# Kernel tuning notes

Hardware: AMD Instinct MI355X
Metric: run time of the kernel (lower is better)

Reference implementation:

```python
import jax, jax.numpy as jnp
import numpy as np

# Dimensions (see shape_source)
B, C, H, W = 8, 3, 256, 256
WIDTH = 32   # FNO width
MODES = 12   # modes1 == modes2
L = 4        # number of FNO layers
GAP = 4      # encoder_de sample_gap
PAD = 9      # trans_net.padding


def _downsample(x):
    # Faithful vectorized form of encoder_de.output: keep indices i % GAP == 0
    # (output size int((N-1)/GAP)+1 == number of multiples of GAP below N).
    return x[:, :, ::GAP, ::GAP]


def _spectral_conv(x, w1, w2):
    # SpectralConv2d: rfft2 -> low-mode complex channel mix -> irfft2
    Hp, Wp = x.shape[-2], x.shape[-1]
    x_ft = jnp.fft.rfft2(x)  # [B, WIDTH, Hp, Wp//2+1] complex64
    out_ft = jnp.zeros((x.shape[0], w1.shape[1], Hp, Wp // 2 + 1), dtype=jnp.complex64)
    out_ft = out_ft.at[:, :, :MODES, :MODES].set(
        jnp.einsum('bixy,ioxy->boxy', x_ft[:, :, :MODES, :MODES], w1))
    out_ft = out_ft.at[:, :, -MODES:, :MODES].set(
        jnp.einsum('bixy,ioxy->boxy', x_ft[:, :, -MODES:, :MODES], w2))
    return jnp.fft.irfft2(out_ft, s=(Hp, Wp))


def _forward(x_en, fc0_w, fc0_b, w1r, w1i, w2r, w2i, pw_w, pw_b,
             fc1_w, fc1_b, fc2_w, fc2_b):
    x_de = _downsample(x_en)
    # fc0 on channels-last, back to channels-first
    x = jnp.einsum('bchw,cd->bdhw', x_en, fc0_w) + fc0_b[None, :, None, None]
    # F.pad(x, [0, PAD, 0, PAD]) pads right/bottom of last two dims
    x = jnp.pad(x, ((0, 0), (0, 0), (0, PAD), (0, PAD)))
    for l in range(L):
        w1 = (w1r[l] + 1j * w1i[l]).astype(jnp.complex64)
        w2 = (w2r[l] + 1j * w2i[l]).astype(jnp.complex64)
        x1 = _spectral_conv(x, w1, w2)
        x2 = jnp.einsum('bihw,oi->bohw', x, pw_w[l]) + pw_b[l][None, :, None, None]
        x = x1 + x2
        if l < L - 1:  # last layer has no activation
            x = jax.nn.gelu(x, approximate=False)  # torch F.gelu default = exact erf
    trans_out = x[..., :-PAD, :-PAD].transpose(0, 2, 3, 1)  # [B,H,W,WIDTH]
    h = jax.nn.gelu(trans_out @ fc1_w + fc1_b, approximate=False)  # [B,H,W,128]
    pred_delta = (h @ fc2_w + fc2_b).transpose(0, 3, 1, 2)          # [B,3,H,W]
    pred = pred_delta + x_en
    pred_de = _downsample(pred)
    return pred_de, x_de, pred, x_en


def setup_inputs() -> dict:
    key = jax.random.key(0)
    ks = jax.random.split(key, 14)
    scale = 1.0 / (WIDTH * WIDTH)
    f32 = jnp.float32
    x_en = jax.random.normal(ks[0], (B, C, H, W), f32)
    ctr = jnp.zeros((B, 1), f32)  # accepted but unused by trans_net.forward
    fc0_w = jax.random.normal(ks[1], (3, WIDTH), f32) * 0.2
    fc0_b = jnp.zeros((WIDTH,), f32)
    # torch.rand(..., dtype=cfloat): uniform [0,1) real and imag parts
    w1r = scale * jax.random.uniform(ks[2], (L, WIDTH, WIDTH, MODES, MODES), f32)
    w1i = scale * jax.random.uniform(ks[3], (L, WIDTH, WIDTH, MODES, MODES), f32)
    w2r = scale * jax.random.uniform(ks[4], (L, WIDTH, WIDTH, MODES, MODES), f32)
    w2i = scale * jax.random.uniform(ks[5], (L, WIDTH, WIDTH, MODES, MODES), f32)
    pw_w = jax.random.normal(ks[6], (L, WIDTH, WIDTH), f32) / np.sqrt(WIDTH)  # 1x1 conv [out,in]
    pw_b = jnp.zeros((L, WIDTH), f32)
    fc1_w = jax.random.normal(ks[7], (WIDTH, 128), f32) / np.sqrt(WIDTH)
    fc1_b = jnp.zeros((128,), f32)
    fc2_w = jax.random.normal(ks[8], (128, 3), f32) / np.sqrt(128.0)
    fc2_b = jnp.zeros((3,), f32)
    return dict(x_en=x_en, ctr=ctr, fc0_w=fc0_w, fc0_b=fc0_b,
                w1r=w1r, w1i=w1i, w2r=w2r, w2i=w2i,
                pw_w=pw_w, pw_b=pw_b, fc1_w=fc1_w, fc1_b=fc1_b,
                fc2_w=fc2_w, fc2_b=fc2_b)


def reference(x_en, ctr, fc0_w, fc0_b, w1r, w1i, w2r, w2i, pw_w, pw_b,
              fc1_w, fc1_b, fc2_w, fc2_b):
    del ctr  # unused in the original trans_net.forward
    return _forward(x_en, fc0_w, fc0_b, w1r, w1i, w2r, w2i, pw_w, pw_b,
                    fc1_w, fc1_b, fc2_w, fc2_b)
```

## Files before the change

kernel.cpp:

```cpp
#include <hip/hip_runtime.h>
#include <math.h>

#define HP 265
#define NPIX 70225
#define ROWF 8480
#define TWO_PI 6.28318530717958647692f

#define OFF_X     0
#define OFF_U     8988800
#define OFF_G     10752640
#define OFF_A     11342464
#define OFF_TFB   12427904
#define OFF_TS    12432512
#define OFF_W1B   12436864
#define OFF_W2B   12438912
#define OFF_PWB   12439936

typedef __attribute__((ext_vector_type(8))) short short8;
typedef __attribute__((ext_vector_type(4))) float f32x4;

__device__ __forceinline__ float gelu_f(float v){
  float x2 = v*v;
  float p  = fmaf(x2, 0.10295597f, 2.30212056f);
  float tn = -v*p;
  float e  = __builtin_amdgcn_exp2f(tn);
  float r  = __builtin_amdgcn_rcpf(1.0f + e);
  return v * r;
}
__device__ __forceinline__ unsigned short f2b(float f){
  unsigned u = __float_as_uint(f);
  u += 0x7FFFu + ((u >> 16) & 1u);
  return (unsigned short)(u >> 16);
}
__device__ __forceinline__ unsigned cvtpk(float lo, float hi){
  unsigned r;
  asm("v_cvt_pk_bf16_f32 %0, %1, %2" : "=v"(r) : "v"(lo), "v"(hi));
  return r;
}

__device__ __forceinline__ void init_body(int idx,
                       unsigned short* __restrict__ Tfb, unsigned short* __restrict__ Ts,
                       unsigned short* __restrict__ w1b, unsigned short* __restrict__ w2b,
                       unsigned short* __restrict__ pwb,
                       const float* __restrict__ fc1w, const float* __restrict__ fc2w,
                       const float* __restrict__ pw_w){
  if (idx < 32*288){
    int m = idx / 288, hc = idx % 288;
    unsigned short v = 0;
    if (m < 26 && hc < 265){
      int k = m >> 1;
      int t = (hc*k) % HP;
      float s, c; sincosf(TWO_PI*(float)t/(float)HP, &s, &c);
      v = f2b((m & 1) ? -s : c);
    }
    Tfb[idx] = v;
  }
  if (idx < 272*32){
    int w = idx >> 5, kap = idx & 31;
    unsigned short v = 0;
    if (w < HP && kap < 24){
      int k = kap >> 1;
      int t = (w*k) % HP;
      float s, c; sincosf(TWO_PI*(float)t/(float)HP, &s, &c);
      const float invN = 1.f/70225.f;
      float val = (!(kap&1)) ? invN*(k==0 ? 1.f : 2.f*c)
                             : ((k==0) ? 0.f : -invN*2.f*s);
      v = f2b(val);
    }
    Ts[idx] = v;
  }
  if (idx < 4096){
    int n = idx >> 5, k = idx & 31;
    w1b[idx] = f2b(fc1w[k*128 + n]);
  }
  if (idx < 2048){
    int n = idx >> 7, k = idx & 127;
    w2b[idx] = (n < 3) ? f2b(fc2w[k*3 + n]) : (unsigned short)0;
  }
  if (idx < 4096)
    pwb[idx] = f2b(pw_w[idx]);
}

__global__ __launch_bounds__(256) void k_fc0(const float* __restrict__ xen,
                                             const float* __restrict__ w0,
                                             const float* __restrict__ b0,
                                             unsigned short* __restrict__ xb,
                                             float* __restrict__ out,
                                             unsigned short* __restrict__ Tfb,
                                             unsigned short* __restrict__ Ts,
                                             unsigned short* __restrict__ w1b,
                                             unsigned short* __restrict__ w2b,
                                             unsigned short* __restrict__ pwb,
                                             const float* __restrict__ fc1w,
                                             const float* __restrict__ fc2w,
                                             const float* __restrict__ pw_w){
  if (blockIdx.x >= 2195){
    init_body((blockIdx.x - 2195)*256 + threadIdx.x, Tfb, Ts, w1b, w2b, pwb,
              fc1w, fc2w, pw_w);
    return;
  }
  int idx = blockIdx.x*256 + threadIdx.x;
  if (idx >= 8*NPIX) return;
  int w = idx % HP; int t = idx / HP; int h = t % HP; int b = t / HP;
  float o32[32];
  if (h < 256 && w < 256){
    const float* xp = xen + (((size_t)b*3)*256 + h)*256 + w;
    float c0 = xp[0], c1 = xp[65536], c2 = xp[131072];
    #pragma unroll
    for (int d = 0; d < 32; ++d)
      o32[d] = b0[d] + c0*w0[d] + c1*w0[32+d] + c2*w0[64+d];
    size_t be = ((size_t)b*3)*65536 + (h<<8) + w;
    out[1769472 + be]          = c0;
    out[1769472 + be + 65536]  = c1;
    out[1769472 + be + 131072] = c2;
    if (((h|w)&3) == 0){
      size_t db = ((size_t)b*3)*4096 + ((h>>2)<<6) + (w>>2);
      out[98304 + db]        = c0;
      out[98304 + db + 4096] = c1;
      out[98304 + db + 8192] = c2;
    }
  } else {
    #pragma unroll
    for (int d = 0; d < 32; ++d) o32[d] = 0.f;
  }
  uint4* dst = (uint4*)(xb + (size_t)idx*32);
  #pragma unroll
  for (int q = 0; q < 4; ++q)
    dst[q] = make_uint4(cvtpk(o32[8*q],o32[8*q+1]),   cvtpk(o32[8*q+2],o32[8*q+3]),
                        cvtpk(o32[8*q+4],o32[8*q+5]), cvtpk(o32[8*q+6],o32[8*q+7]));
}

__global__ __launch_bounds__(256) void k_dftm(const unsigned short* __restrict__ xb,
                                              const unsigned short* __restrict__ Tfb,
                                              float* __restrict__ U32){
  int tid = threadIdx.x;
  int wv = tid>>6, lane = tid&63, lr = lane&15, g = lane>>4, lk = g*8;
  int n0 = blockIdx.x*64;
  int b  = blockIdx.y;
  int n  = n0 + wv*16 + lr;
  const unsigned short* xcol = xb + (size_t)b*HP*ROWF + n;
  f32x4 acc0 = {0.f,0.f,0.f,0.f}, acc1 = {0.f,0.f,0.f,0.f};
  #pragma unroll
  for (int kc = 0; kc < 9; ++kc){
    short8 hv;
    int hb = kc*32 + lk;
    #pragma unroll
    for (int q = 0; q < 8; ++q){
      int h = hb + q;
      hv[q] = (h < HP) ? (short)xcol[(size_t)h*ROWF] : (short)0;
    }
    short8 aT0 = *(const short8*)&Tfb[lr*288 + kc*32 + lk];
    short8 aT1 = *(const short8*)&Tfb[(16+lr)*288 + kc*32 + lk];
    acc0 = __builtin_amdgcn_mfma_f32_16x16x32_bf16(aT0, hv, acc0, 0,0,0);
    acc1 = __builtin_amdgcn_mfma_f32_16x16x32_bf16(aT1, hv, acc1, 0,0,0);
  }
  if (n < 8480){
    #pragma unroll
    for (int r = 0; r < 4; ++r){
      int m0 = g*4 + r;
      U32[((size_t)b*26 + m0)*8480 + n] = acc0[r];
      int m1 = 16 + m0;
      if (m1 < 26) U32[((size_t)b*26 + m1)*8480 + n] = acc1[r];
    }
  }
}

__global__ __launch_bounds__(256) void k_spec(const float* __restrict__ U32,
                                              const float* __restrict__ w1r,
                                              const float* __restrict__ w1i,
                                              const float* __restrict__ w2r,
                                              const float* __restrict__ w2i,
                                              float2* __restrict__ G, int l){
  __shared__ float part[256*25];
  __shared__ float Xs[32*25];
  int j = blockIdx.x;
  int b = blockIdx.y;
  int ws = blockIdx.z;
  int tid = threadIdx.x;
  int wsub = tid >> 5, i = tid & 31;
  int kk   = (j < 12) ? j : (24 - j);
  bool cj  = (j >= 12);
  float xr[12], xi[12];
  #pragma unroll
  for (int k = 0; k < 12; ++k){ xr[k] = 0.f; xi[k] = 0.f; }
  const float* ubr = U32 + ((size_t)(b*26 + 2*kk))*8480;
  for (int w = ws*8 + wsub; w < HP; w += 32){
    int n = w*32 + i;
    float ux = ubr[n];
    float uy = ubr[8480 + n];
    if (cj) uy = -uy;
    float bs, bc; sincosf(-TWO_PI*(float)w/(float)HP, &bs, &bc);
    float pr = 1.f, pi = 0.f;
    #pragma unroll
    for (int k = 0; k < 12; ++k){
      xr[k] = fmaf(ux, pr, fmaf(-uy, pi, xr[k]));
      xi[k] = fmaf(ux, pi, fmaf( uy, pr, xi[k]));
      float npr = pr*bc - pi*bs;
      pi = fmaf(pr, bs, pi*bc);
      pr = npr;
    }
  }
  #pragma unroll
  for (int k = 0; k < 12; ++k){
    part[tid*25 + 2*k]     = xr[k];
    part[tid*25 + 2*k + 1] = xi[k];
  }
  __syncthreads();
  {
    int sg = tid >> 5;
    int ii = tid & 31;
    #pragma unroll
    for (int s0 = 0; s0 < 3; ++s0){
      int s = sg*3 + s0;
      float acc = 0.f;
      #pragma unroll
      for (int wq = 0; wq < 8; ++wq) acc += part[(wq*32 + ii)*25 + s];
      Xs[ii*25 + s] = acc;
    }
  }
  __syncthreads();
  int ky = (j < 12) ? j : (j - 12);
  const float* wr = (j < 12) ? w1r : w2r;
  const float* wi = (j < 12) ? w1i : w2i;
  float2* Gp = G + (size_t)ws*73728;
  for (int p = tid; p < 384; p += 256){
    int o = p / 12, kx = p % 12;
    size_t wbase = (size_t)l*147456 + (size_t)o*144 + (size_t)ky*12 + kx;
    float gr = 0.f, gi = 0.f;
    #pragma unroll 4
    for (int i2 = 0; i2 < 32; ++i2){
      float xvr = Xs[i2*25 + 2*kx];
      float xvi = Xs[i2*25 + 2*kx + 1];
      float a = wr[wbase + (size_t)i2*4608];
      float c = wi[wbase + (size_t)i2*4608];
      gr += xvr*a - xvi*c;
      gi += xvr*c + xvi*a;
    }
    Gp[((size_t)(b*32 + o)*24 + j)*12 + kx] = make_float2(gr, gi);
  }
}

__global__ __launch_bounds__(320) void k_idft_h(const float2* __restrict__ G,
                                                unsigned short* __restrict__ A16){
  __shared__ float2 gs[288];
  int bo = blockIdx.x;
  for (int i = threadIdx.x; i < 288; i += 320){
    float2 g0 = G[(size_t)bo*288 + i];
    float2 g1 = G[73728 + (size_t)bo*288 + i];
    float2 g2 = G[2*73728 + (size_t)bo*288 + i];
    float2 g3 = G[3*73728 + (size_t)bo*288 + i];
    gs[i] = make_float2(g0.x+g1.x+g2.x+g3.x, g0.y+g1.y+g2.y+g3.y);
  }
  __syncthreads();
  if (threadIdx.x >= 133) return;
  int h = blockIdx.y*133 + threadIdx.x;
  if (h >= HP) return;
  float ar[12], ai[12];
  #pragma unroll
  for (int k = 0; k < 12; ++k){ ar[k] = 0.f; ai[k] = 0.f; }
  for (int j = 0; j < 24; ++j){
    int ky = (j < 12) ? j : (241 + j);
    int t = (ky*h) % HP;
    float s, c; sincosf(TWO_PI*(float)t/(float)HP, &s, &c);
    #pragma unroll
    for (int k = 0; k < 12; ++k){
      float2 g = gs[j*12 + k];
      ar[k] = fmaf(g.x, c, fmaf(-g.y, s, ar[k]));
      ai[k] = fmaf(g.x, s, fmaf( g.y, c, ai[k]));
    }
  }
  int b = bo >> 5, o = bo & 31;
  uint4* ap = (uint4*)(A16 + (((size_t)(b*HP + h))*32 + o)*32);
  #pragma unroll
  for (int q = 0; q < 3; ++q)
    ap[q] = make_uint4(cvtpk(ar[4*q],   ai[4*q]),   cvtpk(ar[4*q+1], ai[4*q+1]),
                       cvtpk(ar[4*q+2], ai[4*q+2]), cvtpk(ar[4*q+3], ai[4*q+3]));
  ap[3] = make_uint4(0u, 0u, 0u, 0u);
}

__global__ __launch_bounds__(256) void k_final(const unsigned short* __restrict__ A16,
                                               const unsigned short* __restrict__ Tsyn,
                                               const unsigned short* __restrict__ pwb,
                                               const float* __restrict__ pw_b,
                                               unsigned short* __restrict__ xb, int l){
  int tid = threadIdx.x;
  int wv = tid>>6, lane = tid&63, lr = lane&15, g = lane>>4, lk = g*8;
  int h = blockIdx.x*4 + wv;
  int b = blockIdx.y;
  int z = blockIdx.z;
  if (h >= HP) return;
  const unsigned short* arow = A16 + (size_t)(b*HP + h)*1024;
  short8 aA0 = *(const short8*)&arow[lr*32 + lk];
  short8 aA1 = *(const short8*)&arow[(16+lr)*32 + lk];
  short8 aP0 = *(const short8*)&pwb[l*1024 + lr*32 + lk];
  short8 aP1 = *(const short8*)&pwb[l*1024 + (16+lr)*32 + lk];
  float4 vb0 = *(const float4*)&pw_b[l*32 + g*4];
  float4 vb1 = *(const float4*)&pw_b[l*32 + 16 + g*4];
  unsigned short* xrow = xb + (size_t)(b*HP + h)*ROWF;
  const f32x4 z4 = {0.f,0.f,0.f,0.f};
  const int wt0 = z ? 9 : 0, wt1 = z ? 17 : 9;
  int w = wt0*16 + lr;
  short8 bT = *(const short8*)&Tsyn[(size_t)w*32 + lk];
  short8 bX = *(const short8*)&xrow[(size_t)w*32 + lk];
  #pragma unroll
  for (int wt = wt0; wt < wt1; ++wt){
    short8 nT, nX;
    if (wt + 1 < wt1){
      int wn = (wt+1)*16 + lr;
      nT = *(const short8*)&Tsyn[(size_t)wn*32 + lk];
      nX = *(const short8*)&xrow[(size_t)wn*32 + lk];
    }
    f32x4 a0 = __builtin_amdgcn_mfma_f32_16x16x32_bf16(aA0, bT, z4, 0,0,0);
    a0 = __builtin_amdgcn_mfma_f32_16x16x32_bf16(aP0, bX, a0, 0,0,0);
    f32x4 a1 = __builtin_amdgcn_mfma_f32_16x16x32_bf16(aA1, bT, z4, 0,0,0);
    a1 = __builtin_amdgcn_mfma_f32_16x16x32_bf16(aP1, bX, a1, 0,0,0);
    if (w < HP){
      float v0[4], v1[4];
      v0[0]=a0[0]+vb0.x; v0[1]=a0[1]+vb0.y; v0[2]=a0[2]+vb0.z; v0[3]=a0[3]+vb0.w;
      v1[0]=a1[0]+vb1.x; v1[1]=a1[1]+vb1.y; v1[2]=a1[2]+vb1.z; v1[3]=a1[3]+vb1.w;
      if (l < 3){
        #pragma unroll
        for (int r = 0; r < 4; ++r){ v0[r] = gelu_f(v0[r]); v1[r] = gelu_f(v1[r]); }
      }
      *(uint2*)&xrow[(size_t)w*32 + g*4] =
          make_uint2(cvtpk(v0[0],v0[1]), cvtpk(v0[2],v0[3]));
      *(uint2*)&xrow[(size_t)w*32 + 16 + g*4] =
          make_uint2(cvtpk(v1[0],v1[1]), cvtpk(v1[2],v1[3]));
    }
    bT = nT; bX = nX; w += 16;
  }
}

__global__ __launch_bounds__(256) void k_head(const unsigned short* __restrict__ xb,
                                              const float* __restrict__ xen,
                                              const unsigned short* __restrict__ w1b,
                                              const float* __restrict__ fc1b,
                                              const unsigned short* __restrict__ w2b,
                                              const float* __restrict__ fc2b,
                                              float* __restrict__ out){
  __shared__ unsigned short Pm[4][2][16*136];
  int tid = threadIdx.x;
  int b = blockIdx.x >> 8, h = blockIdx.x & 255;
  int wv = tid>>6, lane = tid&63, lr = lane&15, g = lane>>4, lk = g*8;
  short8 bf1[8], bf2[4];
  #pragma unroll
  for (int nt = 0; nt < 8; ++nt)
    bf1[nt] = *(const short8*)&w1b[(nt*16+lr)*32 + lk];
  #pragma unroll
  for (int ks = 0; ks < 4; ++ks)
    bf2[ks] = *(const short8*)&w2b[lr*128 + ks*32 + lk];
  float f2c = (lr < 3) ? fc2b[lr] : 0.f;
  const unsigned short* xrow = xb + (size_t)(b*HP + h)*ROWF;
  const f32x4 z4 = {0.f,0.f,0.f,0.f};
  #pragma unroll
  for (int m = 0; m < 4; ++m){
    unsigned short* P = Pm[wv][m & 1];
    int p0 = (wv*4 + m)*16;
    short8 ax = *(const short8*)&xrow[(size_t)(p0 + lr)*32 + lk];
    f32x4 acc[8];
    #pragma unroll
    for (int nt = 0; nt < 8; ++nt)
      acc[nt] = __builtin_amdgcn_mfma_f32_16x16x32_bf16(bf1[nt], ax, z4, 0,0,0);
    #pragma unroll
    for (int nt = 0; nt < 8; ++nt){
      float4 bb = *(const float4*)&fc1b[nt*16 + g*4];
      float h0 = gelu_f(acc[nt][0] + bb.x);
      float h1 = gelu_f(acc[nt][1] + bb.y);
      float h2 = gelu_f(acc[nt][2] + bb.z);
      float h3 = gelu_f(acc[nt][3] + bb.w);
      *(uint2*)&P[lr*136 + nt*16 + g*4] =
          make_uint2(cvtpk(h0,h1), cvtpk(h2,h3));
    }
    f32x4 a2 = z4;
    #pragma unroll
    for (int ks = 0; ks < 4; ++ks){
      short8 ap = *(const short8*)&P[lr*136 + ks*32 + lk];
      a2 = __builtin_amdgcn_mfma_f32_16x16x32_bf16(ap, bf2[ks], a2, 0,0,0);
    }
    if (lr < 3){
      size_t base = ((size_t)(b*3 + lr))*65536 + (h<<8) + p0 + g*4;
      float4 xe = *(const float4*)&xen[base];
      float4 pr;
      pr.x = a2[0] + f2c + xe.x;
      pr.y = a2[1] + f2c + xe.y;
      pr.z = a2[2] + f2c + xe.z;
      pr.w = a2[3] + f2c + xe.w;
      *(float4*)&out[196608 + base] = pr;
      if ((h & 3) == 0){
        int w4 = (p0 + g*4) >> 2;
        out[((size_t)(b*3 + lr))*4096 + ((h>>2)<<6) + w4] = pr.x;
      }
    }
  }
}

extern "C" void kernel_launch(void* const* d_in, const int* in_sizes, int n_in,
                              void* d_out, int out_size, void* d_ws, size_t ws_size,
                              hipStream_t stream){
  const float* x_en  = (const float*)d_in[0];
  const float* fc0_w = (const float*)d_in[2];
  const float* fc0_b = (const float*)d_in[3];
  const float* w1r   = (const float*)d_in[4];
  const float* w1i   = (const float*)d_in[5];
  const float* w2r   = (const float*)d_in[6];
  const float* w2i   = (const float*)d_in[7];
  const float* pw_w  = (const float*)d_in[8];
  const float* pw_b  = (const float*)d_in[9];
  const float* fc1_w = (const float*)d_in[10];
  const float* fc1_b = (const float*)d_in[11];
  const float* fc2_w = (const float*)d_in[12];
  const float* fc2_b = (const float*)d_in[13];
  float* out = (float*)d_out;
  float* ws  = (float*)d_ws;

  unsigned short* xb  = (unsigned short*)(ws + OFF_X);
  float*  U32         = ws + OFF_U;
  float2* G           = (float2*)(ws + OFF_G);
  unsigned short* A16 = (unsigned short*)(ws + OFF_A);
  unsigned short* Tfb = (unsigned short*)(ws + OFF_TFB);
  unsigned short* Ts  = (unsigned short*)(ws + OFF_TS);
  unsigned short* w1b = (unsigned short*)(ws + OFF_W1B);
  unsigned short* w2b = (unsigned short*)(ws + OFF_W2B);
  unsigned short* pwb = (unsigned short*)(ws + OFF_PWB);

  k_fc0<<<2231, 256, 0, stream>>>(x_en, fc0_w, fc0_b, xb, out,
                                  Tfb, Ts, w1b, w2b, pwb, fc1_w, fc2_w, pw_w);
  for (int l = 0; l < 4; ++l){
    k_dftm<<<dim3(133,8), 256, 0, stream>>>(xb, Tfb, U32);
    k_spec<<<dim3(24,8,4), 256, 0, stream>>>(U32, w1r, w1i, w2r, w2i, G, l);
    k_idft_h<<<dim3(256,2), 320, 0, stream>>>(G, A16);
    k_final<<<dim3(67,8,2), 256, 0, stream>>>(A16, Ts, pwb, pw_b, xb, l);
  }
  k_head<<<2048, 256, 0, stream>>>(xb, x_en, w1b, fc1_b, w2b, fc2_b, out);
}
```

Before: 302.3 us.

## Fuse last FNO layer's final stage with the projection head

The last layer's spectral-plus-pointwise combine is merged into the head kernel. Its bf16 MFMA output is packed straight into registers as the fc1 operand, so the final activation never goes to global memory and one launch is dropped. To make the accumulator layout line up with the MFMA input fragment, the fc1 weights are stored with a permuted channel order. The new kernel only computes the 256 unpadded rows and columns, skipping the padded region. The cost is a different grid shape and more register pressure in the fused kernel.

```diff
diff --git a/kernel.cpp b/kernel.cpp
--- a/kernel.cpp
+++ b/kernel.cpp
@@ -36,6 +36,11 @@
   unsigned r;
   asm("v_cvt_pk_bf16_f32 %0, %1, %2" : "=v"(r) : "v"(lo), "v"(hi));
   return r;
+}
+__device__ __forceinline__ short8 mk8(unsigned a, unsigned b, unsigned c, unsigned d){
+  union { uint4 u; short8 s; } t;
+  t.u = make_uint4(a, b, c, d);
+  return t.s;
 }
 
 __device__ __forceinline__ void init_body(int idx,
@@ -70,8 +75,10 @@
     Ts[idx] = v;
   }
   if (idx < 4096){
-    int n = idx >> 5, k = idx & 31;
-    w1b[idx] = f2b(fc1w[k*128 + n]);
+    int n = idx >> 5, s = idx & 31;
+    int gg = s >> 3, q = s & 7;
+    int ch = (q < 4) ? (gg*4 + q) : (16 + gg*4 + (q - 4));
+    w1b[idx] = f2b(fc1w[ch*128 + n]);
   }
   if (idx < 2048){
     int n = idx >> 7, k = idx & 127;
@@ -318,10 +325,8 @@
       float v0[4], v1[4];
       v0[0]=a0[0]+vb0.x; v0[1]=a0[1]+vb0.y; v0[2]=a0[2]+vb0.z; v0[3]=a0[3]+vb0.w;
       v1[0]=a1[0]+vb1.x; v1[1]=a1[1]+vb1.y; v1[2]=a1[2]+vb1.z; v1[3]=a1[3]+vb1.w;
-      if (l < 3){
-        #pragma unroll
-        for (int r = 0; r < 4; ++r){ v0[r] = gelu_f(v0[r]); v1[r] = gelu_f(v1[r]); }
-      }
+      #pragma unroll
+      for (int r = 0; r < 4; ++r){ v0[r] = gelu_f(v0[r]); v1[r] = gelu_f(v1[r]); }
       *(uint2*)&xrow[(size_t)w*32 + g*4] =
           make_uint2(cvtpk(v0[0],v0[1]), cvtpk(v0[2],v0[3]));
       *(uint2*)&xrow[(size_t)w*32 + 16 + g*4] =
@@ -331,36 +336,60 @@
   }
 }
 
-__global__ __launch_bounds__(256) void k_head(const unsigned short* __restrict__ xb,
+__global__ __launch_bounds__(256) void k_last(const unsigned short* __restrict__ A16,
+                                              const unsigned short* __restrict__ Tsyn,
+                                              const unsigned short* __restrict__ pwb,
+                                              const float* __restrict__ pw_b,
+                                              const unsigned short* __restrict__ xb,
                                               const float* __restrict__ xen,
-                                              const unsigned short* __restrict__ w1b,
+                                              const unsigned short* __restrict__ w1bp,
                                               const float* __restrict__ fc1b,
                                               const unsigned short* __restrict__ w2b,
                                               const float* __restrict__ fc2b,
                                               float* __restrict__ out){
-  __shared__ unsigned short Pm[4][2][16*136];
+  __shared__ unsigned short Pm[4][16*136];
   int tid = threadIdx.x;
-  int b = blockIdx.x >> 8, h = blockIdx.x & 255;
   int wv = tid>>6, lane = tid&63, lr = lane&15, g = lane>>4, lk = g*8;
+  int h = blockIdx.x*4 + wv;
+  int b = blockIdx.y;
+  int z = blockIdx.z;
+  const int l = 3;
+  const unsigned short* arow = A16 + (size_t)(b*HP + h)*1024;
+  short8 aA0 = *(const short8*)&arow[lr*32 + lk];
+  short8 aA1 = *(const short8*)&arow[(16+lr)*32 + lk];
+  short8 aP0 = *(const short8*)&pwb[l*1024 + lr*32 + lk];
+  short8 aP1 = *(const short8*)&pwb[l*1024 + (16+lr)*32 + lk];
+  float4 vb0 = *(const float4*)&pw_b[l*32 + g*4];
+  float4 vb1 = *(const float4*)&pw_b[l*32 + 16 + g*4];
   short8 bf1[8], bf2[4];
   #pragma unroll
   for (int nt = 0; nt < 8; ++nt)
-    bf1[nt] = *(const short8*)&w1b[(nt*16+lr)*32 + lk];
+    bf1[nt] = *(const short8*)&w1bp[(nt*16+lr)*32 + lk];
   #pragma unroll
   for (int ks = 0; ks < 4; ++ks)
     bf2[ks] = *(const short8*)&w2b[lr*128 + ks*32 + lk];
   float f2c = (lr < 3) ? fc2b[lr] : 0.f;
   const unsigned short* xrow = xb + (size_t)(b*HP + h)*ROWF;
+  unsigned short* P = Pm[wv];
   const f32x4 z4 = {0.f,0.f,0.f,0.f};
-  #pragma unroll
-  for (int m = 0; m < 4; ++m){
-    unsigned short* P = Pm[wv][m & 1];
-    int p0 = (wv*4 + m)*16;
-    short8 ax = *(const short8*)&xrow[(size_t)(p0 + lr)*32 + lk];
+  for (int wt = z*8; wt < z*8 + 8; ++wt){
+    int w0 = wt*16;
+    int w = w0 + lr;
+    short8 bT = *(const short8*)&Tsyn[(size_t)w*32 + lk];
+    short8 bX = *(const short8*)&xrow[(size_t)w*32 + lk];
+    f32x4 a0 = __builtin_amdgcn_mfma_f32_16x16x32_bf16(aA0, bT, z4, 0,0,0);
+    a0 = __builtin_amdgcn_mfma_f32_16x16x32_bf16(aP0, bX, a0, 0,0,0);
+    f32x4 a1 = __builtin_amdgcn_mfma_f32_16x16x32_bf16(aA1, bT, z4, 0,0,0);
+    a1 = __builtin_amdgcn_mfma_f32_16x16x32_bf16(aP1, bX, a1, 0,0,0);
+    float v0[4], v1[4];
+    v0[0]=a0[0]+vb0.x; v0[1]=a0[1]+vb0.y; v0[2]=a0[2]+vb0.z; v0[3]=a0[3]+vb0.w;
+    v1[0]=a1[0]+vb1.x; v1[1]=a1[1]+vb1.y; v1[2]=a1[2]+vb1.z; v1[3]=a1[3]+vb1.w;
+    short8 xf = mk8(cvtpk(v0[0],v0[1]), cvtpk(v0[2],v0[3]),
+                    cvtpk(v1[0],v1[1]), cvtpk(v1[2],v1[3]));
     f32x4 acc[8];
     #pragma unroll
     for (int nt = 0; nt < 8; ++nt)
-      acc[nt] = __builtin_amdgcn_mfma_f32_16x16x32_bf16(bf1[nt], ax, z4, 0,0,0);
+      acc[nt] = __builtin_amdgcn_mfma_f32_16x16x32_bf16(bf1[nt], xf, z4, 0,0,0);
     #pragma unroll
     for (int nt = 0; nt < 8; ++nt){
       float4 bb = *(const float4*)&fc1b[nt*16 + g*4];
@@ -378,7 +407,7 @@
       a2 = __builtin_amdgcn_mfma_f32_16x16x32_bf16(ap, bf2[ks], a2, 0,0,0);
     }
     if (lr < 3){
-      size_t base = ((size_t)(b*3 + lr))*65536 + (h<<8) + p0 + g*4;
+      size_t base = ((size_t)(b*3 + lr))*65536 + (h<<8) + w0 + g*4;
       float4 xe = *(const float4*)&xen[base];
       float4 pr;
       pr.x = a2[0] + f2c + xe.x;
@@ -387,7 +416,7 @@
       pr.w = a2[3] + f2c + xe.w;
       *(float4*)&out[196608 + base] = pr;
       if ((h & 3) == 0){
-        int w4 = (p0 + g*4) >> 2;
+        int w4 = (w0 + g*4) >> 2;
         out[((size_t)(b*3 + lr))*4096 + ((h>>2)<<6) + w4] = pr.x;
       }
     }
@@ -429,7 +458,9 @@
     k_dftm<<<dim3(133,8), 256, 0, stream>>>(xb, Tfb, U32);
     k_spec<<<dim3(24,8,4), 256, 0, stream>>>(U32, w1r, w1i, w2r, w2i, G, l);
     k_idft_h<<<dim3(256,2), 320, 0, stream>>>(G, A16);
-    k_final<<<dim3(67,8,2), 256, 0, stream>>>(A16, Ts, pwb, pw_b, xb, l);
-  }
-  k_head<<<2048, 256, 0, stream>>>(xb, x_en, w1b, fc1_b, w2b, fc2_b, out);
-}
+    if (l < 3)
+      k_final<<<dim3(67,8,2), 256, 0, stream>>>(A16, Ts, pwb, pw_b, xb, l);
+  }
+  k_last<<<dim3(64,8,2), 256, 0, stream>>>(A16, Ts, pwb, pw_b, xb, x_en,
+                                           w1b, fc1_b, w2b, fc2_b, out);
+}
```

After: 282.1 us. 6.7% less time.
